# Performance work log

Hardware: AMD Instinct MI355X
Metric: run time of the kernel (lower is better)

## Reference

```python
import jax, jax.numpy as jnp
import numpy as np

B, N, E, C, K, D, L, FC, IN, OUT = 2, 40000, 320000, 128, 64, 2, 4, 128, 3, 1


def _gelu(x):
    return jax.nn.gelu(x, approximate=False)  # torch F.gelu default = exact erf


def _compute_gradient(f, tgt, src, egw):
    # f: [B,C,N]; tgt,src: [B,E] int; egw: [B,E,D] -> returns [B, C*D, N]
    fT = f.transpose(0, 2, 1)  # [B,N,C]
    diff = jnp.take_along_axis(fT, src[..., None], axis=1) - jnp.take_along_axis(fT, tgt[..., None], axis=1)  # [B,E,C]
    msg = (diff[:, :, :, None] * egw[:, :, None, :]).reshape(fT.shape[0], tgt.shape[1], -1)  # [B,E,C*D], c outer / d inner
    g = jnp.zeros((fT.shape[0], fT.shape[1], msg.shape[-1]), f.dtype)
    g = g.at[jnp.arange(fT.shape[0])[:, None], tgt].add(msg)  # scatter_add over target nodes
    return g.transpose(0, 2, 1)


def _spectral(x, wc, ws, w0, bc, bs, b0, wbc, wbs, wb0):
    # x: [B,Cin,N]; wc/ws: [Cin,Cout,K]; w0: [Cin,Cout,1]; bases: [B,N,K] or [B,N,1]
    xc = jnp.einsum('bix,bxk->bik', x, wbc)
    xs = -jnp.einsum('bix,bxk->bik', x, wbs)
    x0 = jnp.einsum('bix,bxk->bik', x, wb0)
    fc = jnp.einsum('bik,iok->bok', xc, wc) - jnp.einsum('bik,iok->bok', xs, ws)
    fs = jnp.einsum('bik,iok->bok', xs, wc) + jnp.einsum('bik,iok->bok', xc, ws)
    f0 = jnp.einsum('bik,iok->bok', x0, w0)
    return (jnp.einsum('bok,bxk->box', f0, b0)
            + 2.0 * jnp.einsum('bok,bxk->box', fc, bc)
            - 2.0 * jnp.einsum('bok,bxk->box', fs, bs))


def _forward(x, node_mask, nodes, node_weights, edge_gradient_weights, modes,
             fc0_w, fc0_b, sp_wc, sp_ws, sp_w0, w_w, w_b, gw_w, gw_b,
             fc1_w, fc1_b, fc2_w, fc2_b, directed_edges):
    temp = jnp.einsum('bxd,kd->bxk', nodes, modes)
    bc = jnp.cos(temp) * node_mask
    bs = jnp.sin(temp) * node_mask
    b0 = node_mask
    wbc, wbs, wb0 = bc * node_weights, bs * node_weights, b0 * node_weights
    h = (x @ fc0_w + fc0_b).transpose(0, 2, 1)  # lift -> [B,C,N]
    tgt = directed_edges[..., 0]
    src = directed_edges[..., 1]
    nl = sp_wc.shape[0]
    for i in range(nl):
        x1 = _spectral(h, sp_wc[i], sp_ws[i], sp_w0[i], bc, bs, b0, wbc, wbs, wb0)
        x2 = jnp.einsum('oc,bcn->bon', w_w[i], h) + w_b[i][None, :, None]  # 1x1 conv
        # x3 is computed but NOT added, exactly matching the source (x = x1 + x2)
        x3 = jnp.einsum('oc,bcn->bon', gw_w[i],
                        jax.nn.soft_sign(_compute_gradient(h, tgt, src, edge_gradient_weights))) + gw_b[i][None, :, None]
        h = x1 + x2
        if i != nl - 1:
            h = _gelu(h)
    h = h.transpose(0, 2, 1)  # [B,N,C]
    h = _gelu(h @ fc1_w + fc1_b)
    return h @ fc2_w + fc2_b  # [B,N,OUT]


def setup_inputs() -> dict:
    key = jax.random.key(0)
    ks = jax.random.split(key, 16)
    scale = 1.0 / float(C * C)
    return {
        'x': jax.random.normal(ks[0], (B, N, IN), jnp.float32),
        'node_mask': jnp.ones((B, N, 1), jnp.float32),
        'nodes': jax.random.uniform(ks[1], (B, N, D), jnp.float32),
        'node_weights': jax.random.uniform(ks[2], (B, N, 1), jnp.float32) * (1.0 / N),
        'directed_edges': jax.random.randint(ks[3], (B, E, 2), 0, N, dtype=jnp.int32),
        'edge_gradient_weights': jax.random.normal(ks[4], (B, E, D), jnp.float32) * 0.1,
        'modes': jax.random.normal(ks[5], (K, D), jnp.float32) * 4.0,
        'fc0_w': jax.random.normal(ks[6], (IN, C), jnp.float32) * float(1.0 / np.sqrt(IN)),
        'fc0_b': jnp.zeros((C,), jnp.float32),
        'sp_wc': jax.random.uniform(ks[7], (L, C, C, K), jnp.float32) * scale,
        'sp_ws': jax.random.uniform(ks[8], (L, C, C, K), jnp.float32) * scale,
        'sp_w0': jax.random.uniform(ks[9], (L, C, C, 1), jnp.float32) * scale,
        'w_w': jax.random.normal(ks[10], (L, C, C), jnp.float32) * float(1.0 / np.sqrt(C)),
        'w_b': jnp.zeros((L, C), jnp.float32),
        'gw_w': jax.random.normal(ks[11], (L, C, D * C), jnp.float32) * float(1.0 / np.sqrt(D * C)),
        'gw_b': jnp.zeros((L, C), jnp.float32),
        'fc1_w': jax.random.normal(ks[12], (C, FC), jnp.float32) * float(1.0 / np.sqrt(C)),
        'fc1_b': jnp.zeros((FC,), jnp.float32),
        'fc2_w': jax.random.normal(ks[13], (FC, OUT), jnp.float32) * float(1.0 / np.sqrt(FC)),
        'fc2_b': jnp.zeros((OUT,), jnp.float32),
    }


def reference(x, node_mask, nodes, node_weights, directed_edges, edge_gradient_weights, modes,
              fc0_w, fc0_b, sp_wc, sp_ws, sp_w0, w_w, w_b, gw_w, gw_b,
              fc1_w, fc1_b, fc2_w, fc2_b):
    return _forward(x, node_mask, nodes, node_weights, edge_gradient_weights, modes,
                    fc0_w, fc0_b, sp_wc, sp_ws, sp_w0, w_w, w_b, gw_w, gw_b,
                    fc1_w, fc1_b, fc2_w, fc2_b, directed_edges)
```

## Files before the change

### kernel.cpp

```cpp
#include <hip/hip_runtime.h>
#include <math.h>

#define NN 40000
#define NP 40064
#define CC 128
#define KK 64
#define BATCH 2
#define NLAYER 4
#define FSPLITS 128
#define MODES 144
#define KTOT 256
#define NCH 626

typedef __attribute__((ext_vector_type(8))) short bf16x8;
typedef __attribute__((ext_vector_type(4))) float f32x4;
typedef __attribute__((ext_vector_type(4))) unsigned short u16x4;
typedef __attribute__((ext_vector_type(8))) unsigned short u16x8;

__device__ __forceinline__ float gelu_exact(float x) {
    return 0.5f * x * (1.0f + erff(x * 0.70710678118654752f));
}
__device__ __forceinline__ unsigned short f2bf(float x) {
    unsigned int u = __float_as_uint(x);
    u += 0x7FFFu + ((u >> 16) & 1u);
    return (unsigned short)(u >> 16);
}
__device__ __forceinline__ float bf2f(unsigned short v) {
    return __uint_as_float(((unsigned int)v) << 16);
}

__global__ void fc1t_kernel(const float* __restrict__ fc1, unsigned short* __restrict__ fc1t) {
    int idx = blockIdx.x * 256 + threadIdx.x;
    int f = idx >> 7, c = idx & 127;
    fc1t[f * 128 + c] = f2bf(fc1[c * 128 + f]);
}

__global__ __launch_bounds__(512) void lift_fused(const float* __restrict__ x,
        const float* __restrict__ w, const float* __restrict__ bvec,
        const float* __restrict__ nodes, const float* __restrict__ mask,
        const float* __restrict__ wts, const float* __restrict__ modes,
        unsigned short* __restrict__ Binv, float* __restrict__ maskp,
        float* __restrict__ warr, unsigned short* __restrict__ pxcs) {
    int s = blockIdx.x, b = blockIdx.y;
    int t = threadIdx.x, wv = t >> 6, l = t & 63, lo = l & 15, hi = l >> 4;
    __shared__ __align__(16) char lds[53504];
    char* Ts   = lds;
    char* Ts2  = lds + 16384;
    char* Wt   = lds + 32768;
    float* xl  = (float*)(lds + 51200);
    float* ndl = (float*)(lds + 51968);
    float* wl  = (float*)(lds + 52480);
    float* ml  = (float*)(lds + 52736);
    float* sm  = (float*)(lds + 52992);
    int c = t & 127, ng = t >> 7;
    float w0 = w[c], w1 = w[CC + c], w2 = w[2 * CC + c], bv = bvec[c];
    f32x4 accF[9];
    #pragma unroll
    for (int mt = 0; mt < 9; ++mt) accF[mt] = (f32x4){0.f, 0.f, 0.f, 0.f};
    if (t < 128) sm[t] = modes[t];
    if (t < 480) *(unsigned int*)(Wt + 129 * 128 + t * 4) = 0u;

    auto fetch = [&](int chunk) -> float {
        int nbase = chunk * 64;
        if (nbase >= NN) return 0.f;
        long base = (long)b * NN + nbase;
        if (t < 192) return x[base * 3 + t];
        if (t < 320) return nodes[base * 2 + (t - 192)];
        if (t < 384) return wts[base + (t - 320)];
        if (t < 448) return mask[base + (t - 384)];
        return 0.f;
    };
    float pf = fetch(s);

    for (int chunk = s; chunk < NCH; chunk += FSPLITS) {
        int nbase = chunk * 64;
        __syncthreads();
        {
            if (t < 192)      xl[t] = pf;
            else if (t < 320) ndl[t - 192] = pf;
            else if (t < 384) wl[t - 320] = pf;
            else if (t < 448) ml[t - 384] = pf;
        }
        int nc = chunk + FSPLITS;
        if (nc < NCH) pf = fetch(nc);
        __syncthreads();
        {
            int n_ = t & 63, g = t >> 6;
            float nx = ndl[n_ * 2], ny = ndl[n_ * 2 + 1];
            float m = ml[n_];
            u16x8 cosr, sinr;
            #pragma unroll
            for (int j = 0; j < 8; ++j) {
                int k = g * 8 + j;
                float tv = nx * sm[2 * k] + ny * sm[2 * k + 1];
                float sv, cv;
                __sincosf(tv, &sv, &cv);
                unsigned short cb = f2bf(cv * m), sb = f2bf(sv * m);
                cosr[j] = cb; sinr[j] = sb;
                *(unsigned short*)(Wt + ((k * 128 + n_ * 2) ^ ((k & 7) << 4))) = cb;
                *(unsigned short*)(Wt + (((64 + k) * 128 + n_ * 2) ^ (((64 + k) & 7) << 4))) = sb;
            }
            char* brow = (char*)Binv + ((long)b * NP + nbase + n_) * 512 + g * 16;
            *(u16x8*)brow = cosr;
            *(u16x8*)(brow + 128) = sinr;
            if (t < 64) {
                *(unsigned short*)(Wt + 128 * 128 + n_ * 2) = f2bf(m);
                maskp[(long)b * NP + nbase + n_] = m;
                warr[(long)b * NP + nbase + n_] = wl[n_];
            }
        }
        {
            u16x8 hv0, hv1;
            #pragma unroll
            for (int j = 0; j < 16; ++j) {
                int n = ng * 16 + j;
                float h = bv + xl[n * 3] * w0 + xl[n * 3 + 1] * w1 + xl[n * 3 + 2] * w2;
                unsigned short hb = f2bf(h);
                unsigned short hwb = f2bf(h * wl[n]);
                if (j < 8) hv0[j] = hwb; else hv1[j - 8] = hwb;
                *(unsigned short*)(Ts + (((n << 8) + c * 2) ^ ((n & 7) << 4))) = hb;
            }
            int base2 = c * 128 + ng * 32;
            *(u16x8*)(Ts2 + (base2 ^ ((c & 7) << 4))) = hv0;
            *(u16x8*)(Ts2 + ((base2 + 16) ^ ((c & 7) << 4))) = hv1;
        }
        __syncthreads();
        char* Bdst = (char*)Binv + ((long)b * NP + nbase) * 512 + 256;
        #pragma unroll
        for (int pass = 0; pass < 2; ++pass) {
            int n = pass * 32 + (t >> 4), seg = t & 15;
            uint4 v = *(const uint4*)(Ts + (((n << 8) + (seg << 4)) ^ ((n & 7) << 4)));
            *(uint4*)(Bdst + (long)n * 512 + seg * 16) = v;
        }
        int ct = wv * 16;
        #pragma unroll
        for (int ks2 = 0; ks2 < 2; ++ks2) {
            int ar = ct + lo;
            bf16x8 a = *(const bf16x8*)(Ts2 + ((ar * 128 + ks2 * 64 + hi * 16) ^ ((ar & 7) << 4)));
            #pragma unroll
            for (int mt = 0; mt < 9; ++mt) {
                int mrow = mt * 16 + lo;
                bf16x8 bb = *(const bf16x8*)(Wt + ((mrow * 128 + ks2 * 64 + hi * 16) ^ ((mrow & 7) << 4)));
                accF[mt] = __builtin_amdgcn_mfma_f32_16x16x32_bf16(a, bb, accF[mt], 0, 0, 0);
            }
        }
    }
    unsigned short* pb = pxcs + ((long)s * BATCH + b) * CC * MODES;
    #pragma unroll
    for (int mt = 0; mt < 9; ++mt)
        #pragma unroll
        for (int r = 0; r < 4; ++r)
            pb[(long)(wv * 16 + hi * 4 + r) * MODES + mt * 16 + lo] = f2bf(accF[mt][r]);
}

__global__ __launch_bounds__(256) void reduce_kernel(const unsigned short* __restrict__ pxcs,
        float* __restrict__ xc, float* __restrict__ xs, float* __restrict__ x0) {
    int gid = blockIdx.x * 256 + threadIdx.x;
    int idx = gid >> 3, sg = gid & 7;
    float a = 0.f;
    #pragma unroll
    for (int j = 0; j < 16; ++j)
        a += bf2f(pxcs[(long)(sg * 16 + j) * (BATCH * CC * MODES) + idx]);
    a += __shfl_xor(a, 1); a += __shfl_xor(a, 2); a += __shfl_xor(a, 4);
    if (sg == 0) {
        int m = idx % MODES, bc_ = idx / MODES;
        if (m < 64)        xc[bc_ * KK + m] = a;
        else if (m < 128)  xs[bc_ * KK + m - 64] = a;
        else if (m == 128) x0[bc_] = a;
    }
}

__global__ __launch_bounds__(1024) void mix_kernel(const float* __restrict__ xc,
        const float* __restrict__ xs, const float* __restrict__ x0,
        const float* __restrict__ wc, const float* __restrict__ wsp,
        const float* __restrict__ w0, const float* __restrict__ ww,
        const float* __restrict__ wbias, unsigned short* __restrict__ A,
        float* __restrict__ f0a, float* __restrict__ wba, int layer) {
    int o = blockIdx.x, b = blockIdx.y;
    int k = threadIdx.x & 63, ig = threadIdx.x >> 6;
    const float* wcl = wc  + (long)layer * CC * CC * KK;
    const float* wsl = wsp + (long)layer * CC * CC * KK;
    float fc = 0.f, fs = 0.f;
    #pragma unroll
    for (int j = 0; j < 8; ++j) {
        int i = ig * 8 + j;
        float xci = xc[(b * CC + i) * KK + k];
        float xsi = xs[(b * CC + i) * KK + k];
        float wcv = wcl[((long)i * CC + o) * KK + k];
        float wsv = wsl[((long)i * CC + o) * KK + k];
        fc += xci * wcv + xsi * wsv;
        fs += xci * wsv - xsi * wcv;
    }
    __shared__ float rc[16][64], rs[16][64];
    rc[ig][k] = fc; rs[ig][k] = fs;
    __syncthreads();
    unsigned short* Ar = A + ((long)b * CC + o) * KTOT;
    if (ig == 0) {
        fc = 0.f; fs = 0.f;
        #pragma unroll
        for (int j = 0; j < 16; ++j) { fc += rc[j][k]; fs += rs[j][k]; }
        Ar[k]      = f2bf(2.f * fc);
        Ar[64 + k] = f2bf(-2.f * fs);
    } else if (ig == 1) {
        const float* wwl = ww + ((long)layer * CC + o) * CC;
        Ar[128 + k] = f2bf(wwl[k]);
        Ar[192 + k] = f2bf(wwl[64 + k]);
    } else if (ig == 2) {
        const float* w0l = w0 + (long)layer * CC * CC;
        float p = x0[b * CC + k] * w0l[(long)k * CC + o]
                + x0[b * CC + 64 + k] * w0l[(long)(64 + k) * CC + o];
        #pragma unroll
        for (int off = 32; off > 0; off >>= 1) p += __shfl_down(p, off, 64);
        if (k == 0) { f0a[b * CC + o] = p; wba[b * CC + o] = wbias[layer * CC + o]; }
    }
}

template <int DO_FWD, int DOGELU>
__global__ __launch_bounds__(512) void fused_inv(const unsigned short* __restrict__ Amat,
        unsigned short* Binv, const float* __restrict__ f0a, const float* __restrict__ wba,
        const float* __restrict__ maskp, const float* __restrict__ warr,
        unsigned short* __restrict__ pxcs) {
    int s = blockIdx.x, b = blockIdx.y;
    int t = threadIdx.x, wv = t >> 6, l = t & 63, lo = l & 15, hi = l >> 4;
    __shared__ __align__(16) char lds[51712];
    char* Btile = lds;
    char* Ts    = lds;
    char* Ts2   = lds + 16384;
    char* Wt    = lds + 32768;
    float* ml   = (float*)(lds + 51200);
    float* wl   = (float*)(lds + 51456);
    const unsigned short* Ab = Amat + (long)b * CC * KTOT;
    bf16x8 af[8];
    {
        const unsigned short* arow = Ab + (long)(wv * 16 + lo) * KTOT + hi * 8;
        #pragma unroll
        for (int ks = 0; ks < 8; ++ks) af[ks] = *(const bf16x8*)(arow + ks * 32);
    }
    int o0 = wv * 16 + hi * 4;
    f32x4 f0v = *(const f32x4*)(f0a + b * CC + o0);
    f32x4 wbv = *(const f32x4*)(wba + b * CC + o0);
    int swz = (lo & 7) << 4;
    f32x4 accF[9];
    #pragma unroll
    for (int mt = 0; mt < 9; ++mt) accF[mt] = (f32x4){0.f, 0.f, 0.f, 0.f};
    const char* Bbase = (const char*)Binv + (long)b * NP * 512;
    if (DO_FWD && t < 480) *(unsigned int*)(Wt + 129 * 128 + t * 4) = 0u;

    uint4 pB0 = {}, pB1 = {}, pB2 = {}, pB3 = {};
    float pmv = 0.f, pwv = 0.f;
    {
        const char* Bsrc = Bbase + (long)s * 64 * 512;
        pB0 = *(const uint4*)(Bsrc + 0 * 8192 + t * 16);
        pB1 = *(const uint4*)(Bsrc + 1 * 8192 + t * 16);
        pB2 = *(const uint4*)(Bsrc + 2 * 8192 + t * 16);
        pB3 = *(const uint4*)(Bsrc + 3 * 8192 + t * 16);
        if (t < 64) { pmv = maskp[(long)b * NP + s * 64 + t]; pwv = warr[(long)b * NP + s * 64 + t]; }
    }

    for (int chunk = s; chunk < NCH; chunk += FSPLITS) {
        int nbase = chunk * 64;
        __syncthreads();
        {
            int o = 0 * 8192 + t * 16; *(uint4*)(Btile + (o ^ (((o >> 9) & 7) << 4))) = pB0;
            o = 1 * 8192 + t * 16;     *(uint4*)(Btile + (o ^ (((o >> 9) & 7) << 4))) = pB1;
            o = 2 * 8192 + t * 16;     *(uint4*)(Btile + (o ^ (((o >> 9) & 7) << 4))) = pB2;
            o = 3 * 8192 + t * 16;     *(uint4*)(Btile + (o ^ (((o >> 9) & 7) << 4))) = pB3;
            if (t < 64) { ml[t] = pmv; wl[t] = pwv; }
        }
        int nc = chunk + FSPLITS;
        if (nc < NCH) {
            const char* Bsrc = Bbase + (long)nc * 64 * 512;
            pB0 = *(const uint4*)(Bsrc + 0 * 8192 + t * 16);
            pB1 = *(const uint4*)(Bsrc + 1 * 8192 + t * 16);
            pB2 = *(const uint4*)(Bsrc + 2 * 8192 + t * 16);
            pB3 = *(const uint4*)(Bsrc + 3 * 8192 + t * 16);
            if (t < 64) { pmv = maskp[(long)b * NP + nc * 64 + t]; pwv = warr[(long)b * NP + nc * 64 + t]; }
        }
        __syncthreads();
        if (DO_FWD) {
            int g = t >> 6, n_ = t & 63;
            int rkey = (n_ & 7) << 4;
            int raddr = n_ * 512 + g * 32;
            u16x8 r0 = *(const u16x8*)(Btile + (raddr ^ rkey));
            u16x8 r1 = *(const u16x8*)(Btile + ((raddr + 16) ^ rkey));
            #pragma unroll
            for (int i = 0; i < 8; ++i) {
                int mr = g * 16 + i;
                *(unsigned short*)(Wt + ((mr * 128 + n_ * 2) ^ ((mr & 7) << 4))) = r0[i];
            }
            #pragma unroll
            for (int i = 0; i < 8; ++i) {
                int mr = g * 16 + 8 + i;
                *(unsigned short*)(Wt + ((mr * 128 + n_ * 2) ^ ((mr & 7) << 4))) = r1[i];
            }
            if (t < 64) *(unsigned short*)(Wt + 128 * 128 + t * 2) = f2bf(ml[t]);
        }
        f32x4 acc[4];
        #pragma unroll
        for (int fn = 0; fn < 4; ++fn) acc[fn] = (f32x4){0.f, 0.f, 0.f, 0.f};
        #pragma unroll
        for (int ks = 0; ks < 8; ++ks) {
            #pragma unroll
            for (int fn = 0; fn < 4; ++fn) {
                int boff = ((fn * 16 + lo) << 9) + (ks << 6) + (hi << 4);
                bf16x8 bb = *(const bf16x8*)(Btile + (boff ^ swz));
                acc[fn] = __builtin_amdgcn_mfma_f32_16x16x32_bf16(af[ks], bb, acc[fn], 0, 0, 0);
            }
        }
        __syncthreads();
        #pragma unroll
        for (int fn = 0; fn < 4; ++fn) {
            int n = fn * 16 + lo;
            float mv = ml[n];
            u16x4 pk;
            #pragma unroll
            for (int r = 0; r < 4; ++r) {
                float v = acc[fn][r] + f0v[r] * mv + wbv[r];
                if (DOGELU) v = gelu_exact(v);
                pk[r] = f2bf(v);
                if (DO_FWD)
                    *(unsigned short*)(Ts2 + (((o0 + r) * 128 + n * 2) ^ (((o0 + r) & 7) << 4))) = f2bf(v * wl[n]);
            }
            *(u16x4*)(Ts + (((n << 8) + (o0 << 1)) ^ ((n & 7) << 4))) = pk;
        }
        __syncthreads();
        char* Bdst = (char*)Binv + ((long)b * NP + nbase) * 512 + 256;
        #pragma unroll
        for (int pass = 0; pass < 2; ++pass) {
            int n = pass * 32 + (t >> 4), seg = t & 15;
            uint4 v = *(const uint4*)(Ts + (((n << 8) + (seg << 4)) ^ ((n & 7) << 4)));
            *(uint4*)(Bdst + (long)n * 512 + seg * 16) = v;
        }
        if (DO_FWD) {
            int ct = wv * 16;
            #pragma unroll
            for (int ks2 = 0; ks2 < 2; ++ks2) {
                int ar = ct + lo;
                bf16x8 a = *(const bf16x8*)(Ts2 + ((ar * 128 + ks2 * 64 + hi * 16) ^ ((ar & 7) << 4)));
                #pragma unroll
                for (int mt = 0; mt < 9; ++mt) {
                    int mrow = mt * 16 + lo;
                    bf16x8 bb = *(const bf16x8*)(Wt + ((mrow * 128 + ks2 * 64 + hi * 16) ^ ((mrow & 7) << 4)));
                    accF[mt] = __builtin_amdgcn_mfma_f32_16x16x32_bf16(a, bb, accF[mt], 0, 0, 0);
                }
            }
        }
    }
    if (DO_FWD) {
        unsigned short* pb = pxcs + ((long)s * BATCH + b) * CC * MODES;
        #pragma unroll
        for (int mt = 0; mt < 9; ++mt)
            #pragma unroll
            for (int r = 0; r < 4; ++r)
                pb[(long)(wv * 16 + hi * 4 + r) * MODES + mt * 16 + lo] = f2bf(accF[mt][r]);
    }
}

__global__ __launch_bounds__(256) void head_mfma(const unsigned short* __restrict__ Binv,
        const unsigned short* __restrict__ fc1t, const float* __restrict__ b1,
        const float* __restrict__ fc2, const float* __restrict__ b2, float* __restrict__ out) {
    int t = threadIdx.x, wv = t >> 6, l = t & 63, lo = l & 15, hi = l >> 4;
    int b = blockIdx.y;
    int nb = (blockIdx.x * 4 + wv) * 16;
    const unsigned short* Arow = Binv + ((long)b * NP + nb + lo) * KTOT + 128 + hi * 8;
    f32x4 acc[8];
    #pragma unroll
    for (int ft = 0; ft < 8; ++ft) acc[ft] = (f32x4){0.f, 0.f, 0.f, 0.f};
    #pragma unroll
    for (int ks = 0; ks < 4; ++ks) {
        bf16x8 a = *(const bf16x8*)(Arow + ks * 32);
        #pragma unroll
        for (int ft = 0; ft < 8; ++ft) {
            bf16x8 bv = *(const bf16x8*)(fc1t + (ft * 16 + lo) * 128 + ks * 32 + hi * 8);
            acc[ft] = __builtin_amdgcn_mfma_f32_16x16x32_bf16(a, bv, acc[ft], 0, 0, 0);
        }
    }
    float s[4] = {0.f, 0.f, 0.f, 0.f};
    #pragma unroll
    for (int ft = 0; ft < 8; ++ft) {
        int f = ft * 16 + lo;
        float b1f = b1[f], f2f = fc2[f];
        #pragma unroll
        for (int r = 0; r < 4; ++r) s[r] += gelu_exact(acc[ft][r] + b1f) * f2f;
    }
    float b2v = b2[0];
    #pragma unroll
    for (int r = 0; r < 4; ++r) {
        float v = s[r];
        v += __shfl_xor(v, 1); v += __shfl_xor(v, 2);
        v += __shfl_xor(v, 4); v += __shfl_xor(v, 8);
        if (lo == 0) out[(long)b * NN + nb + hi * 4 + r] = v + b2v;
    }
}

extern "C" void kernel_launch(void* const* d_in, const int* in_sizes, int n_in,
                              void* d_out, int out_size, void* d_ws, size_t ws_size,
                              hipStream_t stream) {
    const float* x     = (const float*)d_in[0];
    const float* mask  = (const float*)d_in[1];
    const float* nodes = (const float*)d_in[2];
    const float* wts   = (const float*)d_in[3];
    const float* modes = (const float*)d_in[6];
    const float* fc0w  = (const float*)d_in[7];
    const float* fc0b  = (const float*)d_in[8];
    const float* spwc  = (const float*)d_in[9];
    const float* spws  = (const float*)d_in[10];
    const float* spw0  = (const float*)d_in[11];
    const float* ww    = (const float*)d_in[12];
    const float* wb    = (const float*)d_in[13];
    const float* fc1w  = (const float*)d_in[16];
    const float* fc1b  = (const float*)d_in[17];
    const float* fc2w  = (const float*)d_in[18];
    const float* fc2b  = (const float*)d_in[19];

    char* p = (char*)d_ws;
    auto alloc = [&](size_t bytes) { char* r = p; p += (bytes + 255) & ~255UL; return r; };
    unsigned short* Binv = (unsigned short*)alloc((size_t)BATCH * NP * KTOT * 2);
    unsigned short* Amat = (unsigned short*)alloc((size_t)BATCH * CC * KTOT * 2);
    unsigned short* fc1t = (unsigned short*)alloc((size_t)CC * 128 * 2);
    unsigned short* pxcs = (unsigned short*)alloc((size_t)FSPLITS * BATCH * CC * MODES * 2);
    float* xcb  = (float*)alloc((size_t)BATCH * CC * KK * 4);
    float* xsb  = (float*)alloc((size_t)BATCH * CC * KK * 4);
    float* x0b  = (float*)alloc((size_t)BATCH * CC * 4);
    float* f0a  = (float*)alloc((size_t)BATCH * CC * 4);
    float* wba  = (float*)alloc((size_t)BATCH * CC * 4);
    float* maskp = (float*)alloc((size_t)BATCH * NP * 4);
    float* warr  = (float*)alloc((size_t)BATCH * NP * 4);

    fc1t_kernel<<<64, 256, 0, stream>>>(fc1w, fc1t);
    lift_fused<<<dim3(FSPLITS, BATCH), 512, 0, stream>>>(x, fc0w, fc0b, nodes, mask, wts,
                                                         modes, Binv, maskp, warr, pxcs);

    for (int l = 0; l < NLAYER; ++l) {
        reduce_kernel<<<(8 * BATCH * CC * MODES) / 256, 256, 0, stream>>>(pxcs, xcb, xsb, x0b);
        mix_kernel<<<dim3(CC, BATCH), 1024, 0, stream>>>(xcb, xsb, x0b, spwc, spws, spw0,
                                                         ww, wb, Amat, f0a, wba, l);
        if (l < NLAYER - 1)
            fused_inv<1, 1><<<dim3(FSPLITS, BATCH), 512, 0, stream>>>(
                Amat, Binv, f0a, wba, maskp, warr, pxcs);
        else
            fused_inv<0, 0><<<dim3(FSPLITS, BATCH), 512, 0, stream>>>(
                Amat, Binv, f0a, wba, maskp, warr, pxcs);
    }
    head_mfma<<<dim3(NN / 64, BATCH), 256, 0, stream>>>(Binv, fc1t, fc1b, fc2w, fc2b, (float*)d_out);
}
```

Baseline: 197.2 us.

## Recompute sin/cos bases in each layer instead of storing them in global memory

The cos/sin basis values are no longer precomputed once and written into a 512-byte-per-node global buffer. Each fused_inv layer now recomputes them from nodes, mask and modes with __sincosf, and only the 128-channel hidden state is stored per node. This halves the global buffer traffic read and written by every layer and drops the maskp/warr side arrays, at the cost of extra transcendental math and a little more LDS in each layer.

```diff
diff --git a/kernel.cpp b/kernel.cpp
--- a/kernel.cpp
+++ b/kernel.cpp
@@ -11,6 +11,7 @@
 #define MODES 144
 #define KTOT 256
 #define NCH 626
+#define NVCH 625
 
 typedef __attribute__((ext_vector_type(8))) short bf16x8;
 typedef __attribute__((ext_vector_type(4))) float f32x4;
@@ -39,8 +40,7 @@
         const float* __restrict__ w, const float* __restrict__ bvec,
         const float* __restrict__ nodes, const float* __restrict__ mask,
         const float* __restrict__ wts, const float* __restrict__ modes,
-        unsigned short* __restrict__ Binv, float* __restrict__ maskp,
-        float* __restrict__ warr, unsigned short* __restrict__ pxcs) {
+        unsigned short* __restrict__ Binv, unsigned short* __restrict__ pxcs) {
     int s = blockIdx.x, b = blockIdx.y;
     int t = threadIdx.x, wv = t >> 6, l = t & 63, lo = l & 15, hi = l >> 4;
     __shared__ __align__(16) char lds[53504];
@@ -61,9 +61,8 @@
     if (t < 480) *(unsigned int*)(Wt + 129 * 128 + t * 4) = 0u;
 
     auto fetch = [&](int chunk) -> float {
-        int nbase = chunk * 64;
-        if (nbase >= NN) return 0.f;
-        long base = (long)b * NN + nbase;
+        if (chunk >= NVCH) return 0.f;
+        long base = (long)b * NN + chunk * 64;
         if (t < 192) return x[base * 3 + t];
         if (t < 320) return nodes[base * 2 + (t - 192)];
         if (t < 384) return wts[base + (t - 320)];
@@ -88,26 +87,16 @@
             int n_ = t & 63, g = t >> 6;
             float nx = ndl[n_ * 2], ny = ndl[n_ * 2 + 1];
             float m = ml[n_];
-            u16x8 cosr, sinr;
             #pragma unroll
             for (int j = 0; j < 8; ++j) {
                 int k = g * 8 + j;
                 float tv = nx * sm[2 * k] + ny * sm[2 * k + 1];
                 float sv, cv;
                 __sincosf(tv, &sv, &cv);
-                unsigned short cb = f2bf(cv * m), sb = f2bf(sv * m);
-                cosr[j] = cb; sinr[j] = sb;
-                *(unsigned short*)(Wt + ((k * 128 + n_ * 2) ^ ((k & 7) << 4))) = cb;
-                *(unsigned short*)(Wt + (((64 + k) * 128 + n_ * 2) ^ (((64 + k) & 7) << 4))) = sb;
-            }
-            char* brow = (char*)Binv + ((long)b * NP + nbase + n_) * 512 + g * 16;
-            *(u16x8*)brow = cosr;
-            *(u16x8*)(brow + 128) = sinr;
-            if (t < 64) {
-                *(unsigned short*)(Wt + 128 * 128 + n_ * 2) = f2bf(m);
-                maskp[(long)b * NP + nbase + n_] = m;
-                warr[(long)b * NP + nbase + n_] = wl[n_];
-            }
+                *(unsigned short*)(Wt + ((k * 128 + n_ * 2) ^ ((k & 7) << 4))) = f2bf(cv * m);
+                *(unsigned short*)(Wt + (((64 + k) * 128 + n_ * 2) ^ (((64 + k) & 7) << 4))) = f2bf(sv * m);
+            }
+            if (t < 64) *(unsigned short*)(Wt + 128 * 128 + n_ * 2) = f2bf(m);
         }
         {
             u16x8 hv0, hv1;
@@ -125,12 +114,12 @@
             *(u16x8*)(Ts2 + ((base2 + 16) ^ ((c & 7) << 4))) = hv1;
         }
         __syncthreads();
-        char* Bdst = (char*)Binv + ((long)b * NP + nbase) * 512 + 256;
+        char* Bdst = (char*)Binv + ((long)b * NP + nbase) * 256;
         #pragma unroll
         for (int pass = 0; pass < 2; ++pass) {
             int n = pass * 32 + (t >> 4), seg = t & 15;
             uint4 v = *(const uint4*)(Ts + (((n << 8) + (seg << 4)) ^ ((n & 7) << 4)));
-            *(uint4*)(Bdst + (long)n * 512 + seg * 16) = v;
+            *(uint4*)(Bdst + (long)n * 256 + seg * 16) = v;
         }
         int ct = wv * 16;
         #pragma unroll
@@ -218,17 +207,20 @@
 template <int DO_FWD, int DOGELU>
 __global__ __launch_bounds__(512) void fused_inv(const unsigned short* __restrict__ Amat,
         unsigned short* Binv, const float* __restrict__ f0a, const float* __restrict__ wba,
-        const float* __restrict__ maskp, const float* __restrict__ warr,
+        const float* __restrict__ nodes, const float* __restrict__ mask,
+        const float* __restrict__ wts, const float* __restrict__ modes,
         unsigned short* __restrict__ pxcs) {
     int s = blockIdx.x, b = blockIdx.y;
     int t = threadIdx.x, wv = t >> 6, l = t & 63, lo = l & 15, hi = l >> 4;
-    __shared__ __align__(16) char lds[51712];
+    __shared__ __align__(16) char lds[52736];
     char* Btile = lds;
     char* Ts    = lds;
     char* Ts2   = lds + 16384;
     char* Wt    = lds + 32768;
-    float* ml   = (float*)(lds + 51200);
-    float* wl   = (float*)(lds + 51456);
+    float* ndl  = (float*)(lds + 51200);
+    float* wl   = (float*)(lds + 51712);
+    float* ml   = (float*)(lds + 51968);
+    float* sm   = (float*)(lds + 52224);
     const unsigned short* Ab = Amat + (long)b * CC * KTOT;
     bf16x8 af[8];
     {
@@ -243,58 +235,71 @@
     f32x4 accF[9];
     #pragma unroll
     for (int mt = 0; mt < 9; ++mt) accF[mt] = (f32x4){0.f, 0.f, 0.f, 0.f};
-    const char* Bbase = (const char*)Binv + (long)b * NP * 512;
+    const char* Bbase = (const char*)Binv + (long)b * NP * 256;
+    if (t < 128) sm[t] = modes[t];
     if (DO_FWD && t < 480) *(unsigned int*)(Wt + 129 * 128 + t * 4) = 0u;
 
-    uint4 pB0 = {}, pB1 = {}, pB2 = {}, pB3 = {};
-    float pmv = 0.f, pwv = 0.f;
+    auto fetch = [&](int chunk) -> float {
+        if (chunk >= NVCH) return 0.f;
+        long base = (long)b * NN + chunk * 64;
+        if (t < 128) return nodes[base * 2 + t];
+        if (t < 192) return wts[base + (t - 128)];
+        if (t < 256) return mask[base + (t - 192)];
+        return 0.f;
+    };
+    uint4 pH0 = {}, pH1 = {};
+    float pf;
     {
-        const char* Bsrc = Bbase + (long)s * 64 * 512;
-        pB0 = *(const uint4*)(Bsrc + 0 * 8192 + t * 16);
-        pB1 = *(const uint4*)(Bsrc + 1 * 8192 + t * 16);
-        pB2 = *(const uint4*)(Bsrc + 2 * 8192 + t * 16);
-        pB3 = *(const uint4*)(Bsrc + 3 * 8192 + t * 16);
-        if (t < 64) { pmv = maskp[(long)b * NP + s * 64 + t]; pwv = warr[(long)b * NP + s * 64 + t]; }
+        const char* Hsrc = Bbase + (long)s * 64 * 256;
+        pH0 = *(const uint4*)(Hsrc + t * 16);
+        pH1 = *(const uint4*)(Hsrc + 8192 + t * 16);
+        pf = fetch(s);
     }
 
     for (int chunk = s; chunk < NCH; chunk += FSPLITS) {
         int nbase = chunk * 64;
         __syncthreads();
         {
-            int o = 0 * 8192 + t * 16; *(uint4*)(Btile + (o ^ (((o >> 9) & 7) << 4))) = pB0;
-            o = 1 * 8192 + t * 16;     *(uint4*)(Btile + (o ^ (((o >> 9) & 7) << 4))) = pB1;
-            o = 2 * 8192 + t * 16;     *(uint4*)(Btile + (o ^ (((o >> 9) & 7) << 4))) = pB2;
-            o = 3 * 8192 + t * 16;     *(uint4*)(Btile + (o ^ (((o >> 9) & 7) << 4))) = pB3;
-            if (t < 64) { ml[t] = pmv; wl[t] = pwv; }
+            int o1 = t * 16; int n1 = o1 >> 8;
+            *(uint4*)(Btile + ((n1 * 512 + 256 + (o1 & 255)) ^ ((n1 & 7) << 4))) = pH0;
+            int o2 = 8192 + t * 16; int n2 = o2 >> 8;
+            *(uint4*)(Btile + ((n2 * 512 + 256 + (o2 & 255)) ^ ((n2 & 7) << 4))) = pH1;
+            if (t < 128)      ndl[t] = pf;
+            else if (t < 192) wl[t - 128] = pf;
+            else if (t < 256) ml[t - 192] = pf;
         }
         int nc = chunk + FSPLITS;
         if (nc < NCH) {
-            const char* Bsrc = Bbase + (long)nc * 64 * 512;
-            pB0 = *(const uint4*)(Bsrc + 0 * 8192 + t * 16);
-            pB1 = *(const uint4*)(Bsrc + 1 * 8192 + t * 16);
-            pB2 = *(const uint4*)(Bsrc + 2 * 8192 + t * 16);
-            pB3 = *(const uint4*)(Bsrc + 3 * 8192 + t * 16);
-            if (t < 64) { pmv = maskp[(long)b * NP + nc * 64 + t]; pwv = warr[(long)b * NP + nc * 64 + t]; }
-        }
-        __syncthreads();
-        if (DO_FWD) {
-            int g = t >> 6, n_ = t & 63;
-            int rkey = (n_ & 7) << 4;
-            int raddr = n_ * 512 + g * 32;
-            u16x8 r0 = *(const u16x8*)(Btile + (raddr ^ rkey));
-            u16x8 r1 = *(const u16x8*)(Btile + ((raddr + 16) ^ rkey));
-            #pragma unroll
-            for (int i = 0; i < 8; ++i) {
-                int mr = g * 16 + i;
-                *(unsigned short*)(Wt + ((mr * 128 + n_ * 2) ^ ((mr & 7) << 4))) = r0[i];
-            }
-            #pragma unroll
-            for (int i = 0; i < 8; ++i) {
-                int mr = g * 16 + 8 + i;
-                *(unsigned short*)(Wt + ((mr * 128 + n_ * 2) ^ ((mr & 7) << 4))) = r1[i];
-            }
-            if (t < 64) *(unsigned short*)(Wt + 128 * 128 + t * 2) = f2bf(ml[t]);
-        }
+            const char* Hsrc = Bbase + (long)nc * 64 * 256;
+            pH0 = *(const uint4*)(Hsrc + t * 16);
+            pH1 = *(const uint4*)(Hsrc + 8192 + t * 16);
+            pf = fetch(nc);
+        }
+        __syncthreads();
+        {
+            int n_ = t & 63, g = t >> 6;
+            float nx = ndl[n_ * 2], ny = ndl[n_ * 2 + 1];
+            float m = ml[n_];
+            u16x8 cosr, sinr;
+            #pragma unroll
+            for (int j = 0; j < 8; ++j) {
+                int k = g * 8 + j;
+                float tv = nx * sm[2 * k] + ny * sm[2 * k + 1];
+                float sv, cv;
+                __sincosf(tv, &sv, &cv);
+                unsigned short cb = f2bf(cv * m), sb = f2bf(sv * m);
+                cosr[j] = cb; sinr[j] = sb;
+                if (DO_FWD) {
+                    *(unsigned short*)(Wt + ((k * 128 + n_ * 2) ^ ((k & 7) << 4))) = cb;
+                    *(unsigned short*)(Wt + (((64 + k) * 128 + n_ * 2) ^ (((64 + k) & 7) << 4))) = sb;
+                }
+            }
+            int key = (n_ & 7) << 4;
+            *(u16x8*)(Btile + ((n_ * 512 + g * 16) ^ key)) = cosr;
+            *(u16x8*)(Btile + ((n_ * 512 + 128 + g * 16) ^ key)) = sinr;
+            if (DO_FWD && t < 64) *(unsigned short*)(Wt + 128 * 128 + n_ * 2) = f2bf(m);
+        }
+        __syncthreads();
         f32x4 acc[4];
         #pragma unroll
         for (int fn = 0; fn < 4; ++fn) acc[fn] = (f32x4){0.f, 0.f, 0.f, 0.f};
@@ -324,12 +329,12 @@
             *(u16x4*)(Ts + (((n << 8) + (o0 << 1)) ^ ((n & 7) << 4))) = pk;
         }
         __syncthreads();
-        char* Bdst = (char*)Binv + ((long)b * NP + nbase) * 512 + 256;
+        char* Bdst = (char*)Binv + ((long)b * NP + nbase) * 256;
         #pragma unroll
         for (int pass = 0; pass < 2; ++pass) {
             int n = pass * 32 + (t >> 4), seg = t & 15;
             uint4 v = *(const uint4*)(Ts + (((n << 8) + (seg << 4)) ^ ((n & 7) << 4)));
-            *(uint4*)(Bdst + (long)n * 512 + seg * 16) = v;
+            *(uint4*)(Bdst + (long)n * 256 + seg * 16) = v;
         }
         if (DO_FWD) {
             int ct = wv * 16;
@@ -362,7 +367,7 @@
     int t = threadIdx.x, wv = t >> 6, l = t & 63, lo = l & 15, hi = l >> 4;
     int b = blockIdx.y;
     int nb = (blockIdx.x * 4 + wv) * 16;
-    const unsigned short* Arow = Binv + ((long)b * NP + nb + lo) * KTOT + 128 + hi * 8;
+    const unsigned short* Arow = Binv + ((long)b * NP + nb + lo) * 128 + hi * 8;
     f32x4 acc[8];
     #pragma unroll
     for (int ft = 0; ft < 8; ++ft) acc[ft] = (f32x4){0.f, 0.f, 0.f, 0.f};
@@ -415,7 +420,7 @@
 
     char* p = (char*)d_ws;
     auto alloc = [&](size_t bytes) { char* r = p; p += (bytes + 255) & ~255UL; return r; };
-    unsigned short* Binv = (unsigned short*)alloc((size_t)BATCH * NP * KTOT * 2);
+    unsigned short* Binv = (unsigned short*)alloc((size_t)BATCH * NP * 128 * 2);
     unsigned short* Amat = (unsigned short*)alloc((size_t)BATCH * CC * KTOT * 2);
     unsigned short* fc1t = (unsigned short*)alloc((size_t)CC * 128 * 2);
     unsigned short* pxcs = (unsigned short*)alloc((size_t)FSPLITS * BATCH * CC * MODES * 2);
@@ -424,12 +429,10 @@
     float* x0b  = (float*)alloc((size_t)BATCH * CC * 4);
     float* f0a  = (float*)alloc((size_t)BATCH * CC * 4);
     float* wba  = (float*)alloc((size_t)BATCH * CC * 4);
-    float* maskp = (float*)alloc((size_t)BATCH * NP * 4);
-    float* warr  = (float*)alloc((size_t)BATCH * NP * 4);
 
     fc1t_kernel<<<64, 256, 0, stream>>>(fc1w, fc1t);
     lift_fused<<<dim3(FSPLITS, BATCH), 512, 0, stream>>>(x, fc0w, fc0b, nodes, mask, wts,
-                                                         modes, Binv, maskp, warr, pxcs);
+                                                         modes, Binv, pxcs);
 
     for (int l = 0; l < NLAYER; ++l) {
         reduce_kernel<<<(8 * BATCH * CC * MODES) / 256, 256, 0, stream>>>(pxcs, xcb, xsb, x0b);
@@ -437,10 +440,10 @@
                                                          ww, wb, Amat, f0a, wba, l);
         if (l < NLAYER - 1)
             fused_inv<1, 1><<<dim3(FSPLITS, BATCH), 512, 0, stream>>>(
-                Amat, Binv, f0a, wba, maskp, warr, pxcs);
+                Amat, Binv, f0a, wba, nodes, mask, wts, modes, pxcs);
         else
             fused_inv<0, 0><<<dim3(FSPLITS, BATCH), 512, 0, stream>>>(
-                Amat, Binv, f0a, wba, maskp, warr, pxcs);
+                Amat, Binv, f0a, wba, nodes, mask, wts, modes, pxcs);
     }
     head_mfma<<<dim3(NN / 64, BATCH), 256, 0, stream>>>(Binv, fc1t, fc1b, fc2w, fc2b, (float*)d_out);
 }
```

New measurement: 205.8 us. 4.4% more time.
